# Kernel tuning notes

Hardware: AMD Instinct MI355X
Metric: run time of the kernel (lower is better)

Reference implementation:

```python
import jax, jax.numpy as jnp
import numpy as np

DIM = 1024
NUM_HEADS = 8
HEAD_DIM = 128
MAX_SEQ_LEN = 2048
ATTN_SCALE = 0.12
RMS_EPS = 1.1920929e-07  # torch float32 eps (F.rms_norm default)


def rms_norm(x):
    return x * jax.lax.rsqrt(jnp.mean(jnp.square(x), axis=-1, keepdims=True) + RMS_EPS)


def rope_tables(T):
    # angular_freq: (1/1024)**linspace(0,1,head_dim//4), padded with head_dim//4 zeros -> length head_dim//2
    af = (1.0 / 1024.0) ** np.linspace(0.0, 1.0, HEAD_DIM // 4, dtype=np.float32)
    af = np.concatenate([af, np.zeros(HEAD_DIM // 4, dtype=np.float32)])
    t = np.arange(T, dtype=np.float32)
    theta = np.einsum('i,j->ij', t, af)  # [T, head_dim//2]
    return jnp.asarray(np.cos(theta)), jnp.asarray(np.sin(theta))


def apply_rope(x_BTHD, cos, sin):
    # cos/sin: [T, head_dim//2] -> broadcast [1,T,1,hd//2]
    c = cos[None, :, None, :]
    s = sin[None, :, None, :]
    x1, x2 = jnp.split(x_BTHD, 2, axis=-1)
    y1 = x1 * c + x2 * s
    y2 = -x1 * s + x2 * c
    return jnp.concatenate([y1, y2], axis=-1)


def setup_inputs() -> dict:
    key = jax.random.key(0)
    k1, k2, k3, k4, k5 = jax.random.split(key, 5)
    B, T = 4, 2048
    hdim = NUM_HEADS * HEAD_DIM
    std = 0.5 * DIM ** (-0.5)
    bound = (3.0 ** 0.5) * std
    x = jax.random.normal(k1, (B, T, DIM), dtype=jnp.float32)
    ve = jax.random.normal(k2, (B, T, DIM), dtype=jnp.float32)
    sa_lambdas = jax.random.uniform(k3, (2,), dtype=jnp.float32)
    qkv_w = jax.random.uniform(k4, (3, hdim, DIM), dtype=jnp.float32, minval=-bound, maxval=bound)
    # original inits c_proj to zeros; use small random so the output is non-trivial
    c_proj_weight = jax.random.normal(k5, (DIM, hdim), dtype=jnp.float32) * 0.02
    return {"x": x, "ve": ve, "sa_lambdas": sa_lambdas, "qkv_w": qkv_w,
            "c_proj_weight": c_proj_weight}


def reference(x, ve, sa_lambdas, qkv_w, c_proj_weight):
    B, T, D = x.shape
    H, hd = NUM_HEADS, HEAD_DIM
    Wqkv = qkv_w.reshape(3 * H * hd, D)
    qkv = jnp.einsum('btd,ed->bte', x, Wqkv).reshape(B, T, 3 * H, hd)
    q, k, v = jnp.split(qkv, 3, axis=-2)  # each [B,T,H,hd]
    q, k = rms_norm(q), rms_norm(k)
    cos, sin = rope_tables(T)
    q, k = apply_rope(q, cos, sin), apply_rope(k, cos, sin)
    v = sa_lambdas[0] * v + sa_lambdas[1] * ve.reshape(B, T, H, hd)
    # [B,H,T,T] scores
    attn = jnp.einsum('bqhd,bkhd->bhqk', q, k) * ATTN_SCALE
    causal = jnp.triu(jnp.ones((T, T), dtype=bool), k=1)
    attn = jnp.where(causal[None, None], -jnp.inf, attn)
    attn = jax.nn.softmax(attn, axis=-1)
    y = jnp.einsum('bhqk,bkhd->bqhd', attn, v).reshape(B, T, H * hd)
    return jnp.einsum('bte,de->btd', y, c_proj_weight)
```

## Files before the change

kernel.cpp:

```cpp
#include <hip/hip_runtime.h>

#define DIM 1024
#define NH 8
#define HD 128
#define T_SEQ 2048
#define NTOK 8192
#define QKV_N 3072
#define ATTN_SCALE 0.12f
#define RMS_EPS 1.1920929e-07f

using f32x4  = __attribute__((ext_vector_type(4))) float;
using bf16x8 = __attribute__((ext_vector_type(8))) __bf16;

__device__ __forceinline__ unsigned short f2bf(float f) {
    unsigned int u = __builtin_bit_cast(unsigned int, f);
    u += 0x7fffu + ((u >> 16) & 1u);
    return (unsigned short)(u >> 16);
}
__device__ __forceinline__ float bf2f(unsigned short s) {
    unsigned int u = ((unsigned int)s) << 16;
    return __builtin_bit_cast(float, u);
}
__device__ __forceinline__ unsigned int cvtpk(float lo, float hi) {
    unsigned int r;
    asm("v_cvt_pk_bf16_f32 %0, %1, %2" : "=v"(r) : "v"(lo), "v"(hi));
    return r;
}

__device__ __forceinline__ void gll16(const void* g, void* l) {
    __builtin_amdgcn_global_load_lds(
        (const __attribute__((address_space(1))) unsigned int*)g,
        (__attribute__((address_space(3))) unsigned int*)l, 16, 0, 0);
}

#define VMCNT(n) asm volatile("s_waitcnt vmcnt(" #n ")" ::: "memory")
#define LGKM(n)  asm volatile("s_waitcnt lgkmcnt(" #n ")" ::: "memory")
#define LGKM0 do { asm volatile("s_waitcnt lgkmcnt(0)" ::: "memory"); \
                   __builtin_amdgcn_sched_barrier(0); } while(0)
#define PH_BAR __builtin_amdgcn_s_barrier()

__global__ __launch_bounds__(256) void prep(const float* __restrict__ x,
                                            const float* __restrict__ qkvw,
                                            const float* __restrict__ cprojw,
                                            unsigned short* __restrict__ xb,
                                            unsigned short* __restrict__ wqb,
                                            unsigned short* __restrict__ cpb,
                                            float2* __restrict__ tab) {
    const int bid = blockIdx.x;
    const int tid = threadIdx.x;
    if (bid < 12288) {
        const float* in;
        unsigned short* out;
        int i;
        if (bid < 8192)        { in = x;      out = xb;  i = bid*256 + tid; }
        else if (bid < 11264)  { in = qkvw;   out = wqb; i = (bid-8192)*256 + tid; }
        else                   { in = cprojw; out = cpb; i = (bid-11264)*256 + tid; }
        float4 f = ((const float4*)in)[i];
        ushort4 o;
        o.x = f2bf(f.x); o.y = f2bf(f.y); o.z = f2bf(f.z); o.w = f2bf(f.w);
        ((ushort4*)out)[i] = o;
    } else {
        int idx = (bid - 12288)*256 + tid;
        int t = idx >> 5, i = idx & 31;
        float th = (float)t * exp2f((float)i * (-10.0f/31.0f));
        float sn, cs;
        sincosf(th, &sn, &cs);
        tab[idx] = make_float2(cs, sn);
    }
}

template<int OUTF32>
__global__ __launch_bounds__(512, 2) void gemm8p(const unsigned short* __restrict__ A,
                                                 const unsigned short* __restrict__ B,
                                                 void* __restrict__ Cout,
                                                 int M, int N, int K, int nbn) {
    __shared__ __align__(16) char smem[139264];
    const int tid  = threadIdx.x;
    const int lane = tid & 63;
    const int w    = tid >> 6;
    const int wm   = w >> 2, wn = w & 3;
    const int lr   = lane & 15, lg = lane >> 4;

    const int chunk = gridDim.x >> 3;
    const int bid2  = (blockIdx.x & 7) * chunk + (blockIdx.x >> 3);
    const int bm = (bid2 / nbn) * 256;
    const int bn = (bid2 % nbn) * 256;

    const int rsub = lane >> 3;
    const int csw  = ((lane & 7) ^ rsub) << 3;
    const int KT = K / 64;

    auto stA = [&](int t, int h) {
        if (t >= KT) return;
        char* dst = smem + (t & 1) * 65536 + h * 16384;
        #pragma unroll
        for (int i = 0; i < 2; ++i) {
            int c = w*2 + i;
            gll16(&A[(size_t)(bm + h*128 + c*8 + rsub)*K + t*64 + csw], dst + c*1024);
        }
    };
    auto stB = [&](int t, int h) {
        if (t >= KT) return;
        char* dst = smem + (t & 1) * 65536 + 32768 + h * 16384;
        #pragma unroll
        for (int i = 0; i < 2; ++i) {
            int c = w*2 + i;
            gll16(&B[(size_t)(bn + h*128 + c*8 + rsub)*K + t*64 + csw], dst + c*1024);
        }
    };

    f32x4 acc[8][4] = {};
    bf16x8 a0[4][2], a1[4][2], bb[2][2];

    auto rdA = [&](int t, int qm, bf16x8 (*a)[2]) {
        const unsigned short* base = (const unsigned short*)(smem + (t & 1)*65536 + wm*16384);
        #pragma unroll
        for (int m = 0; m < 4; ++m) {
            int row = qm*64 + m*16 + lr;
            int sw = (row & 7) << 3;
            #pragma unroll
            for (int kk = 0; kk < 2; ++kk)
                a[m][kk] = *(const bf16x8*)&base[row*64 + ((kk*32 + lg*8) ^ sw)];
        }
    };
    auto rdB = [&](int t, int qn) {
        const unsigned short* base = (const unsigned short*)(smem + (t & 1)*65536 + 32768 + (wn >> 1)*16384);
        #pragma unroll
        for (int n = 0; n < 2; ++n) {
            int row = (wn & 1)*64 + qn*32 + n*16 + lr;
            int sw = (row & 7) << 3;
            #pragma unroll
            for (int kk = 0; kk < 2; ++kk)
                bb[n][kk] = *(const bf16x8*)&base[row*64 + ((kk*32 + lg*8) ^ sw)];
        }
    };
    auto mm = [&](bf16x8 (*a)[2], int qm, int qn) {
        __builtin_amdgcn_s_setprio(1);
        #pragma unroll
        for (int m = 0; m < 4; ++m)
            #pragma unroll
            for (int n = 0; n < 2; ++n)
                #pragma unroll
                for (int kk = 0; kk < 2; ++kk)
                    acc[qm*4+m][qn*2+n] =
                        __builtin_amdgcn_mfma_f32_16x16x32_bf16(a[m][kk], bb[n][kk],
                                                                acc[qm*4+m][qn*2+n], 0, 0, 0);
        __builtin_amdgcn_s_setprio(0);
    };

    stA(0, 0); stA(0, 1); stB(0, 0); stB(0, 1);
    stA(1, 0); stA(1, 1);
    VMCNT(4);
    PH_BAR;

    for (int t = 0; t < KT; ++t) {
        rdA(t, 0, a0); rdB(t, 0);
        stB(t + 1, 0);
        LGKM(8);
        PH_BAR; LGKM0;
        mm(a0, 0, 0);
        PH_BAR;
        rdA(t, 1, a1);
        stB(t + 1, 1);
        PH_BAR; LGKM0;
        mm(a1, 1, 0);
        PH_BAR;
        rdB(t, 1);
        stA(t + 2, 0);
        PH_BAR; LGKM0;
        mm(a0, 0, 1);
        PH_BAR;
        stA(t + 2, 1);
        if (t + 2 < KT) { VMCNT(4); } else { VMCNT(0); }
        PH_BAR;
        mm(a1, 1, 1);
        PH_BAR;
    }

    __syncthreads();
    float* sc = (float*)(smem + (size_t)w * 17408);
    #pragma unroll
    for (int f = 0; f < 2; ++f) {
        #pragma unroll
        for (int m = 0; m < 4; ++m)
            #pragma unroll
            for (int n = 0; n < 4; ++n)
                #pragma unroll
                for (int r = 0; r < 4; ++r)
                    sc[(m*16 + lg*4 + r)*68 + n*16 + lr] = acc[f*4+m][n][r];
        if (OUTF32) {
            float* C = (float*)Cout;
            #pragma unroll
            for (int rnd = 0; rnd < 16; ++rnd) {
                int g = rnd*64 + lane;
                int row = g >> 4, c4 = (g & 15) * 4;
                float4 v = *(float4*)&sc[row*68 + c4];
                *(float4*)&C[(size_t)(bm + wm*128 + f*64 + row)*N + bn + wn*64 + c4] = v;
            }
        } else {
            unsigned short* C = (unsigned short*)Cout;
            #pragma unroll
            for (int rnd = 0; rnd < 8; ++rnd) {
                int g = rnd*64 + lane;
                int row = g >> 3, c8 = (g & 7) * 8;
                float4 v0 = *(float4*)&sc[row*68 + c8];
                float4 v1 = *(float4*)&sc[row*68 + c8 + 4];
                uint4 o;
                o.x = f2bf(v0.x) | ((unsigned)f2bf(v0.y) << 16);
                o.y = f2bf(v0.z) | ((unsigned)f2bf(v0.w) << 16);
                o.z = f2bf(v1.x) | ((unsigned)f2bf(v1.y) << 16);
                o.w = f2bf(v1.z) | ((unsigned)f2bf(v1.w) << 16);
                *(uint4*)&C[(size_t)(bm + wm*128 + f*64 + row)*N + bn + wn*64 + c8] = o;
            }
        }
        if (f == 0) __syncthreads();
    }
}

#define SLOT_A 32768
#define SLOT_SZ 49152

template<int OUTF32>
__global__ __launch_bounds__(512, 1) void gemm256(const unsigned short* __restrict__ A,
                                                  const unsigned short* __restrict__ B,
                                                  void* __restrict__ Cout,
                                                  int M, int N, int K, int nbn) {
    __shared__ __align__(16) char smem[147456];
    const int tid  = threadIdx.x;
    const int lane = tid & 63;
    const int w    = tid >> 6;
    const int wm   = w >> 1, wn = w & 1;
    const int lr   = lane & 15, lg = lane >> 4;
    const int xsw  = (lr & 7) << 3;

    const int chunk = gridDim.x >> 3;
    const int bid2  = (blockIdx.x & 7) * chunk + (blockIdx.x >> 3);
    const int m0 = (bid2 / nbn) * 256;
    const int n0 = (bid2 % nbn) * 128;

    const int rsub = lane >> 3;
    const int csw  = ((lane & 7) ^ rsub) << 3;

    char* s0 = smem;
    char* s1 = smem + SLOT_SZ;
    char* s2 = smem + 2*SLOT_SZ;

    auto stage = [&](int kt, char* slot) {
        const int kb = kt * 64;
        #pragma unroll
        for (int i = 0; i < 4; ++i) {
            int c = w*4 + i;
            gll16(&A[(size_t)(m0 + c*8 + rsub)*K + kb + csw], slot + c*1024);
        }
        #pragma unroll
        for (int i = 0; i < 2; ++i) {
            int c = w*2 + i;
            gll16(&B[(size_t)(n0 + c*8 + rsub)*K + kb + csw], slot + SLOT_A + c*1024);
        }
    };

    f32x4 acc[4][4] = {};
    const int KT = K / 64;

    stage(0, s0);
    stage(1, s1);
    VMCNT(6);
    __builtin_amdgcn_s_barrier();
    __builtin_amdgcn_sched_barrier(0);

    for (int t = 0; t < KT; ++t) {
        if (t + 2 < KT) stage(t + 2, s2);
        const unsigned short* sA = (const unsigned short*)s0;
        const unsigned short* sB = (const unsigned short*)(s0 + SLOT_A);
        bf16x8 bfr[4][2];
        #pragma unroll
        for (int n = 0; n < 4; ++n)
            #pragma unroll
            for (int kk = 0; kk < 2; ++kk)
                bfr[n][kk] = *(const bf16x8*)&sB[(wn*64 + n*16 + lr)*64 + ((kk*32 + lg*8) ^ xsw)];
        #pragma unroll
        for (int m = 0; m < 4; ++m) {
            bf16x8 af[2];
            #pragma unroll
            for (int kk = 0; kk < 2; ++kk)
                af[kk] = *(const bf16x8*)&sA[(wm*64 + m*16 + lr)*64 + ((kk*32 + lg*8) ^ xsw)];
            __builtin_amdgcn_s_setprio(1);
            #pragma unroll
            for (int n = 0; n < 4; ++n)
                #pragma unroll
                for (int kk = 0; kk < 2; ++kk)
                    acc[m][n] = __builtin_amdgcn_mfma_f32_16x16x32_bf16(af[kk], bfr[n][kk], acc[m][n], 0, 0, 0);
            __builtin_amdgcn_s_setprio(0);
        }
        if (t + 2 < KT) { VMCNT(6); }
        else            { VMCNT(0); }
        __builtin_amdgcn_s_barrier();
        __builtin_amdgcn_sched_barrier(0);
        char* tmp = s0; s0 = s1; s1 = s2; s2 = tmp;
    }

    __syncthreads();
    float* sc = (float*)(smem + (size_t)w * 17408);
    #pragma unroll
    for (int m = 0; m < 4; ++m)
        #pragma unroll
        for (int n = 0; n < 4; ++n)
            #pragma unroll
            for (int r = 0; r < 4; ++r)
                sc[(m*16 + lg*4 + r)*68 + n*16 + lr] = acc[m][n][r];

    if (OUTF32) {
        float* Cg = (float*)Cout;
        #pragma unroll
        for (int rnd = 0; rnd < 16; ++rnd) {
            int g = rnd*64 + lane;
            int row = g >> 4, c4 = (g & 15) * 4;
            float4 v = *(float4*)&sc[row*68 + c4];
            *(float4*)&Cg[(size_t)(m0 + wm*64 + row)*N + n0 + wn*64 + c4] = v;
        }
    } else {
        unsigned short* Cg = (unsigned short*)Cout;
        #pragma unroll
        for (int rnd = 0; rnd < 8; ++rnd) {
            int g = rnd*64 + lane;
            int row = g >> 3, c8 = (g & 7) * 8;
            float4 v0 = *(float4*)&sc[row*68 + c8];
            float4 v1 = *(float4*)&sc[row*68 + c8 + 4];
            uint4 o;
            o.x = f2bf(v0.x) | ((unsigned)f2bf(v0.y) << 16);
            o.y = f2bf(v0.z) | ((unsigned)f2bf(v0.w) << 16);
            o.z = f2bf(v1.x) | ((unsigned)f2bf(v1.y) << 16);
            o.w = f2bf(v1.z) | ((unsigned)f2bf(v1.w) << 16);
            *(uint4*)&Cg[(size_t)(m0 + wm*64 + row)*N + n0 + wn*64 + c8] = o;
        }
    }
}

__global__ __launch_bounds__(256) void post(const unsigned short* __restrict__ qkv,
                                            const float* __restrict__ ve,
                                            const float* __restrict__ lam,
                                            const float2* __restrict__ tab,
                                            unsigned short* __restrict__ qO,
                                            unsigned short* __restrict__ kO,
                                            unsigned short* __restrict__ vt) {
    __shared__ unsigned short lT[128*72];
    const int bid = blockIdx.x;
    const int tid = threadIdx.x;
    if (bid < 16384) {
        int gw   = (bid*256 + tid) >> 6;
        int lane = tid & 63;
        int h     = gw & 7;
        int token = gw >> 3;
        int t     = token & (T_SEQ-1);
        int b     = token >> 11;

        const unsigned short* base = qkv + (size_t)token * QKV_N + h*HD;
        float q1 = bf2f(base[lane]),        q2 = bf2f(base[lane+64]);
        float k1 = bf2f(base[1024+lane]),   k2 = bf2f(base[1024+lane+64]);

        float sq = q1*q1 + q2*q2;
        float sk = k1*k1 + k2*k2;
        #pragma unroll
        for (int m = 1; m < 64; m <<= 1) {
            sq += __shfl_xor(sq, m);
            sk += __shfl_xor(sk, m);
        }
        float qs = rsqrtf(sq * (1.0f/128.0f) + RMS_EPS) * (ATTN_SCALE * 1.44269504088896f);
        float ks = rsqrtf(sk * (1.0f/128.0f) + RMS_EPS);
        q1 *= qs; q2 *= qs; k1 *= ks; k2 *= ks;

        float cs = 1.0f, sn = 0.0f;
        if (lane < 32) { float2 cc = tab[t*32 + lane]; cs = cc.x; sn = cc.y; }
        float qy1 =  q1*cs + q2*sn, qy2 = -q1*sn + q2*cs;
        float ky1 =  k1*cs + k2*sn, ky2 = -k1*sn + k2*cs;

        size_t obase = ((size_t)(b*NH + h) * T_SEQ + t) * HD;
        qO[obase + lane]      = f2bf(qy1);
        qO[obase + lane + 64] = f2bf(qy2);
        kO[obase + lane]      = f2bf(ky1);
        kO[obase + lane + 64] = f2bf(ky2);
    } else {
        const int idx = bid - 16384;
        const int t0  = (idx & 31) * 64;
        const int bh  = idx >> 5;
        const int b = bh >> 3, h = bh & 7;
        const float l0 = lam[0], l1 = lam[1];
        #pragma unroll
        for (int it = 0; it < 4; ++it) {
            int g  = it*256 + tid;
            int t  = g >> 4;
            int d8 = (g & 15) << 3;
            size_t token = (size_t)b*T_SEQ + t0 + t;
            ushort4 v0 = *(const ushort4*)&qkv[token*QKV_N + 2048 + h*HD + d8];
            ushort4 v1 = *(const ushort4*)&qkv[token*QKV_N + 2048 + h*HD + d8 + 4];
            float4 e0 = *(const float4*)&ve[token*DIM + h*HD + d8];
            float4 e1 = *(const float4*)&ve[token*DIM + h*HD + d8 + 4];
            lT[(d8+0)*72 + t] = f2bf(l0*bf2f(v0.x) + l1*e0.x);
            lT[(d8+1)*72 + t] = f2bf(l0*bf2f(v0.y) + l1*e0.y);
            lT[(d8+2)*72 + t] = f2bf(l0*bf2f(v0.z) + l1*e0.z);
            lT[(d8+3)*72 + t] = f2bf(l0*bf2f(v0.w) + l1*e0.w);
            lT[(d8+4)*72 + t] = f2bf(l0*bf2f(v1.x) + l1*e1.x);
            lT[(d8+5)*72 + t] = f2bf(l0*bf2f(v1.y) + l1*e1.y);
            lT[(d8+6)*72 + t] = f2bf(l0*bf2f(v1.z) + l1*e1.z);
            lT[(d8+7)*72 + t] = f2bf(l0*bf2f(v1.w) + l1*e1.w);
        }
        __syncthreads();
        #pragma unroll
        for (int it = 0; it < 4; ++it) {
            int g  = it*256 + tid;
            int d  = g >> 3;
            int t8 = (g & 7) << 3;
            uint4 pk = *(const uint4*)&lT[d*72 + t8];
            *(uint4*)&vt[((size_t)bh*HD + d)*T_SEQ + t0 + t8] = pk;
        }
    }
}

__global__ __launch_bounds__(256, 2) void attn_fwd(const unsigned short* __restrict__ Q,
                                                   const unsigned short* __restrict__ K,
                                                   const unsigned short* __restrict__ Vt,
                                                   unsigned short* __restrict__ Y) {
    __shared__ unsigned short lK[2][64*128];
    __shared__ unsigned short lV[2][128*64];
    __shared__ unsigned short lP[4][16*72];
    __shared__ float lden[4][2][16];

    const int tid  = threadIdx.x;
    const int lane = tid & 63;
    const int w    = tid >> 6;
    const int lr   = lane & 15, lg = lane >> 4;

    const int lin = blockIdx.y * 16 + blockIdx.x;
    const int bh  = (lin & 7)*4 + ((lin >> 3) & 3);
    const int p   = lin >> 5;
    const int qtA = p, qtB = 31 - p;

    const unsigned short* Qg = Q  + (size_t)bh * T_SEQ * HD;
    const unsigned short* Kg = K  + (size_t)bh * T_SEQ * HD;
    const unsigned short* Vg = Vt + (size_t)bh * HD * T_SEQ;
    const int q0A = qtA*64 + w*16;
    const int q0B = qtB*64 + w*16;

    auto stage = [&](int kt, int s) {
        const int kbase = kt * 64;
        #pragma unroll
        for (int i = 0; i < 4; ++i) {
            int c = w*4 + i;
            int row = c*4 + (lane >> 4);
            int col = ((lane & 15) << 3) ^ ((row & 7) << 3);
            gll16(&Kg[(size_t)(kbase + row)*HD + col], &lK[s][c*512]);
        }
        #pragma unroll
        for (int i = 0; i < 4; ++i) {
            int c = w*4 + i;
            int row = c*8 + (lane >> 3);
            int col = ((lane & 7) << 3) ^ ((row & 7) << 3);
            gll16(&Vg[(size_t)row*T_SEQ + kbase + col], &lV[s][c*512]);
        }
    };

    bf16x8 qfA[4], qfB[4];
    #pragma unroll
    for (int kk = 0; kk < 4; ++kk) {
        qfA[kk] = *(const bf16x8*)&Qg[(size_t)(q0A + lr)*HD + kk*32 + lg*8];
        qfB[kk] = *(const bf16x8*)&Qg[(size_t)(q0B + lr)*HD + kk*32 + lg*8];
    }
    VMCNT(0);
    #pragma unroll
    for (int kk = 0; kk < 4; ++kk)
        asm volatile("" :: "v"(qfA[kk]), "v"(qfB[kk]));

    f32x4 oA[8] = {}, oB[8] = {};
    float psA = 0.f, psB = 0.f;

    auto softmax_pack = [&](f32x4* sf, float& ps, uint2* pk) {
        #pragma unroll
        for (int j = 0; j < 4; ++j)
            #pragma unroll
            for (int r = 0; r < 4; ++r) {
                float pp = exp2f(sf[j][r]);
                sf[j][r] = pp;
                ps += pp;
            }
        #pragma unroll
        for (int j = 0; j < 4; ++j) {
            pk[j].x = cvtpk(sf[j][0], sf[j][1]);
            pk[j].y = cvtpk(sf[j][2], sf[j][3]);
        }
    };
    auto p_store = [&](uint2* pk) {
        #pragma unroll
        for (int j = 0; j < 4; ++j)
            *(uint2*)&lP[w][lr*72 + j*16 + lg*4] = pk[j];
        asm volatile("" ::: "memory");
    };

    auto passAB = [&](bool diagA, int kbase,
                      const unsigned short* lKc, const unsigned short* lVc) {
        f32x4 sfA[4], sfB[4];
        __builtin_amdgcn_s_setprio(1);
        #pragma unroll
        for (int j = 0; j < 4; ++j) {
            f32x4 sA = {0.f,0.f,0.f,0.f}, sB = {0.f,0.f,0.f,0.f};
            #pragma unroll
            for (int kk = 0; kk < 4; ++kk) {
                bf16x8 kf = *(const bf16x8*)&lKc[(j*16+lr)*128 + ((kk*32 + lg*8) ^ ((lr&7)<<3))];
                sA = __builtin_amdgcn_mfma_f32_16x16x32_bf16(kf, qfA[kk], sA, 0, 0, 0);
                sB = __builtin_amdgcn_mfma_f32_16x16x32_bf16(kf, qfB[kk], sB, 0, 0, 0);
            }
            sfA[j] = sA; sfB[j] = sB;
        }
        __builtin_amdgcn_s_setprio(0);
        if (diagA) {
            #pragma unroll
            for (int j = 0; j < 4; ++j)
                #pragma unroll
                for (int r = 0; r < 4; ++r) {
                    int kcol = kbase + j*16 + lg*4 + r;
                    int qrow = q0A + lr;
                    if (kcol > qrow) sfA[j][r] = -INFINITY;
                }
        }
        uint2 pkA[4], pkB[4];
        softmax_pack(sfA, psA, pkA);
        p_store(pkA);
        softmax_pack(sfB, psB, pkB);
        bf16x8 pfA[2];
        #pragma unroll
        for (int kk = 0; kk < 2; ++kk)
            pfA[kk] = *(const bf16x8*)&lP[w][lr*72 + kk*32 + lg*8];
        asm volatile("" ::: "memory");
        p_store(pkB);
        bf16x8 pfB[2];
        #pragma unroll
        for (int kk = 0; kk < 2; ++kk)
            pfB[kk] = *(const bf16x8*)&lP[w][lr*72 + kk*32 + lg*8];
        #pragma unroll
        for (int n = 0; n < 8; ++n) {
            bf16x8 vf0 = *(const bf16x8*)&lVc[(n*16+lr)*64 + (( 0 + lg*8) ^ ((lr&7)<<3))];
            bf16x8 vf1 = *(const bf16x8*)&lVc[(n*16+lr)*64 + ((32 + lg*8) ^ ((lr&7)<<3))];
            __builtin_amdgcn_s_setprio(1);
            oA[n] = __builtin_amdgcn_mfma_f32_16x16x32_bf16(pfA[0], vf0, oA[n], 0, 0, 0);
            oB[n] = __builtin_amdgcn_mfma_f32_16x16x32_bf16(pfB[0], vf0, oB[n], 0, 0, 0);
            oA[n] = __builtin_amdgcn_mfma_f32_16x16x32_bf16(pfA[1], vf1, oA[n], 0, 0, 0);
            oB[n] = __builtin_amdgcn_mfma_f32_16x16x32_bf16(pfB[1], vf1, oB[n], 0, 0, 0);
            __builtin_amdgcn_s_setprio(0);
        }
    };

    auto pass = [&](bool diag, int kbase,
                    const unsigned short* lKc, const unsigned short* lVc) {
        f32x4 sf[4];
        __builtin_amdgcn_s_setprio(1);
        #pragma unroll
        for (int j = 0; j < 4; ++j) {
            f32x4 s = {0.f,0.f,0.f,0.f};
            #pragma unroll
            for (int kk = 0; kk < 4; ++kk) {
                bf16x8 kf = *(const bf16x8*)&lKc[(j*16+lr)*128 + ((kk*32 + lg*8) ^ ((lr&7)<<3))];
                s = __builtin_amdgcn_mfma_f32_16x16x32_bf16(kf, qfB[kk], s, 0, 0, 0);
            }
            sf[j] = s;
        }
        __builtin_amdgcn_s_setprio(0);
        if (diag) {
            #pragma unroll
            for (int j = 0; j < 4; ++j)
                #pragma unroll
                for (int r = 0; r < 4; ++r) {
                    int kcol = kbase + j*16 + lg*4 + r;
                    int qrow = q0B + lr;
                    if (kcol > qrow) sf[j][r] = -INFINITY;
                }
        }
        uint2 pk[4];
        softmax_pack(sf, psB, pk);
        p_store(pk);
        bf16x8 pf[2];
        #pragma unroll
        for (int kk = 0; kk < 2; ++kk)
            pf[kk] = *(const bf16x8*)&lP[w][lr*72 + kk*32 + lg*8];
        #pragma unroll
        for (int n = 0; n < 8; ++n) {
            bf16x8 vf0 = *(const bf16x8*)&lVc[(n*16+lr)*64 + (( 0 + lg*8) ^ ((lr&7)<<3))];
            bf16x8 vf1 = *(const bf16x8*)&lVc[(n*16+lr)*64 + ((32 + lg*8) ^ ((lr&7)<<3))];
            __builtin_amdgcn_s_setprio(1);
            oB[n] = __builtin_amdgcn_mfma_f32_16x16x32_bf16(pf[0], vf0, oB[n], 0, 0, 0);
            oB[n] = __builtin_amdgcn_mfma_f32_16x16x32_bf16(pf[1], vf1, oB[n], 0, 0, 0);
            __builtin_amdgcn_s_setprio(0);
        }
    };

    stage(0, 0);
    for (int kt = 0; kt <= qtB; ++kt) {
        __builtin_amdgcn_s_barrier();
        const bool pre = (kt + 1 <= qtB);
        if (pre) stage(kt + 1, (kt + 1) & 1);
        if (pre) { VMCNT(8); } else { VMCNT(0); }
        __builtin_amdgcn_sched_barrier(0);
        const int kbase = kt * 64;
        const unsigned short* lKc = lK[kt & 1];
        const unsigned short* lVc = lV[kt & 1];
        if (kt <= qtA) passAB(kt == qtA, kbase, lKc, lVc);
        else           pass(kt == qtB, kbase, lKc, lVc);
    }

    psA += __shfl_xor(psA, 16); psA += __shfl_xor(psA, 32);
    psB += __shfl_xor(psB, 16); psB += __shfl_xor(psB, 32);
    if (lane < 16) { lden[w][0][lane] = psA; lden[w][1][lane] = psB; }
    asm volatile("" ::: "memory");
    float riA[4], riB[4];
    #pragma unroll
    for (int r = 0; r < 4; ++r) {
        riA[r] = 1.0f / lden[w][0][lg*4 + r];
        riB[r] = 1.0f / lden[w][1][lg*4 + r];
    }

    const int b = bh >> 3, h = bh & 7;
    #pragma unroll
    for (int n = 0; n < 8; ++n)
        #pragma unroll
        for (int r = 0; r < 4; ++r) {
            int d = n*16 + lr;
            int qrowA = q0A + lg*4 + r;
            int qrowB = q0B + lg*4 + r;
            Y[((size_t)(b*T_SEQ + qrowA))*DIM + h*HD + d] = f2bf(oA[n][r] * riA[r]);
            Y[((size_t)(b*T_SEQ + qrowB))*DIM + h*HD + d] = f2bf(oB[n][r] * riB[r]);
        }
}

extern "C" void kernel_launch(void* const* d_in, const int* in_sizes, int n_in,
                              void* d_out, int out_size, void* d_ws, size_t ws_size,
                              hipStream_t stream) {
    const float* x      = (const float*)d_in[0];
    const float* ve     = (const float*)d_in[1];
    const float* lam    = (const float*)d_in[2];
    const float* qkvw   = (const float*)d_in[3];
    const float* cprojw = (const float*)d_in[4];

    char* ws = (char*)d_ws;
    unsigned short* xb  = (unsigned short*)(ws);
    unsigned short* wqb = (unsigned short*)(ws + 16777216);
    unsigned short* cpb = (unsigned short*)(ws + 23068672);
    unsigned short* qkv = (unsigned short*)(ws + 25165824);
    unsigned short* qa  = (unsigned short*)(ws + 75497472);
    unsigned short* ka  = (unsigned short*)(ws + 92274688);
    unsigned short* vt  = (unsigned short*)(ws + 109051904);
    unsigned short* ya  = (unsigned short*)(ws + 125829120);
    float2* tab = (float2*)(ws + 142606336);

    prep<<<12544, 256, 0, stream>>>(x, qkvw, cprojw, xb, wqb, cpb, tab);

    gemm8p<0><<<384, 512, 0, stream>>>(xb, wqb, qkv, NTOK, QKV_N, DIM, 12);
    post<<<17408, 256, 0, stream>>>(qkv, ve, lam, tab, qa, ka, vt);
    attn_fwd<<<dim3(16, 32), 256, 0, stream>>>(qa, ka, vt, ya);
    gemm256<1><<<256, 512, 0, stream>>>(ya, cpb, (float*)d_out, NTOK, DIM, DIM, 8);
}
```

Before: 190.2 us.

## Stage K/V through registers into single LDS buffer to raise occupancy

Replaces the double-buffered direct global-to-LDS loads of K and V tiles with a single LDS buffer fed from register staging: the next tile is loaded into registers during compute and written to LDS after a barrier. This halves K/V shared memory so launch bounds are raised from 2 to 3 blocks per CU. It costs extra VGPRs for staging, two barriers per iteration, and serializes the LDS write with compute, and the tighter register budget may cause spills.

```diff
diff --git a/kernel.cpp b/kernel.cpp
--- a/kernel.cpp
+++ b/kernel.cpp
@@ -416,12 +416,12 @@
     }
 }
 
-__global__ __launch_bounds__(256, 2) void attn_fwd(const unsigned short* __restrict__ Q,
+__global__ __launch_bounds__(256, 3) void attn_fwd(const unsigned short* __restrict__ Q,
                                                    const unsigned short* __restrict__ K,
                                                    const unsigned short* __restrict__ Vt,
                                                    unsigned short* __restrict__ Y) {
-    __shared__ unsigned short lK[2][64*128];
-    __shared__ unsigned short lV[2][128*64];
+    __shared__ unsigned short lK[64*128];
+    __shared__ unsigned short lV[128*64];
     __shared__ unsigned short lP[4][16*72];
     __shared__ float lden[4][2][16];
 
@@ -441,22 +441,36 @@
     const int q0A = qtA*64 + w*16;
     const int q0B = qtB*64 + w*16;
 
-    auto stage = [&](int kt, int s) {
+    uint4 kst[4], vst[4];
+    auto loadRegs = [&](int kt) {
         const int kbase = kt * 64;
         #pragma unroll
         for (int i = 0; i < 4; ++i) {
             int c = w*4 + i;
             int row = c*4 + (lane >> 4);
             int col = ((lane & 15) << 3) ^ ((row & 7) << 3);
-            gll16(&Kg[(size_t)(kbase + row)*HD + col], &lK[s][c*512]);
+            kst[i] = *(const uint4*)&Kg[(size_t)(kbase + row)*HD + col];
         }
         #pragma unroll
         for (int i = 0; i < 4; ++i) {
             int c = w*4 + i;
             int row = c*8 + (lane >> 3);
             int col = ((lane & 7) << 3) ^ ((row & 7) << 3);
-            gll16(&Vg[(size_t)row*T_SEQ + kbase + col], &lV[s][c*512]);
-        }
+            vst[i] = *(const uint4*)&Vg[(size_t)row*T_SEQ + kbase + col];
+        }
+    };
+    auto writeRegs = [&]() {
+        #pragma unroll
+        for (int i = 0; i < 4; ++i) {
+            int c = w*4 + i;
+            *(uint4*)&lK[c*512 + lane*8] = kst[i];
+        }
+        #pragma unroll
+        for (int i = 0; i < 4; ++i) {
+            int c = w*4 + i;
+            *(uint4*)&lV[c*512 + lane*8] = vst[i];
+        }
+        asm volatile("" ::: "memory");
     };
 
     bf16x8 qfA[4], qfB[4];
@@ -495,8 +509,7 @@
         asm volatile("" ::: "memory");
     };
 
-    auto passAB = [&](bool diagA, int kbase,
-                      const unsigned short* lKc, const unsigned short* lVc) {
+    auto passAB = [&](bool diagA, int kbase) {
         f32x4 sfA[4], sfB[4];
         __builtin_amdgcn_s_setprio(1);
         #pragma unroll
@@ -504,7 +517,7 @@
             f32x4 sA = {0.f,0.f,0.f,0.f}, sB = {0.f,0.f,0.f,0.f};
             #pragma unroll
             for (int kk = 0; kk < 4; ++kk) {
-                bf16x8 kf = *(const bf16x8*)&lKc[(j*16+lr)*128 + ((kk*32 + lg*8) ^ ((lr&7)<<3))];
+                bf16x8 kf = *(const bf16x8*)&lK[(j*16+lr)*128 + ((kk*32 + lg*8) ^ ((lr&7)<<3))];
                 sA = __builtin_amdgcn_mfma_f32_16x16x32_bf16(kf, qfA[kk], sA, 0, 0, 0);
                 sB = __builtin_amdgcn_mfma_f32_16x16x32_bf16(kf, qfB[kk], sB, 0, 0, 0);
             }
@@ -537,8 +550,8 @@
             pfB[kk] = *(const bf16x8*)&lP[w][lr*72 + kk*32 + lg*8];
         #pragma unroll
         for (int n = 0; n < 8; ++n) {
-            bf16x8 vf0 = *(const bf16x8*)&lVc[(n*16+lr)*64 + (( 0 + lg*8) ^ ((lr&7)<<3))];
-            bf16x8 vf1 = *(const bf16x8*)&lVc[(n*16+lr)*64 + ((32 + lg*8) ^ ((lr&7)<<3))];
+            bf16x8 vf0 = *(const bf16x8*)&lV[(n*16+lr)*64 + (( 0 + lg*8) ^ ((lr&7)<<3))];
+            bf16x8 vf1 = *(const bf16x8*)&lV[(n*16+lr)*64 + ((32 + lg*8) ^ ((lr&7)<<3))];
             __builtin_amdgcn_s_setprio(1);
             oA[n] = __builtin_amdgcn_mfma_f32_16x16x32_bf16(pfA[0], vf0, oA[n], 0, 0, 0);
             oB[n] = __builtin_amdgcn_mfma_f32_16x16x32_bf16(pfB[0], vf0, oB[n], 0, 0, 0);
@@ -548,8 +561,7 @@
         }
     };
 
-    auto pass = [&](bool diag, int kbase,
-                    const unsigned short* lKc, const unsigned short* lVc) {
+    auto pass = [&](bool diag, int kbase) {
         f32x4 sf[4];
         __builtin_amdgcn_s_setprio(1);
         #pragma unroll
@@ -557,7 +569,7 @@
             f32x4 s = {0.f,0.f,0.f,0.f};
             #pragma unroll
             for (int kk = 0; kk < 4; ++kk) {
-                bf16x8 kf = *(const bf16x8*)&lKc[(j*16+lr)*128 + ((kk*32 + lg*8) ^ ((lr&7)<<3))];
+                bf16x8 kf = *(const bf16x8*)&lK[(j*16+lr)*128 + ((kk*32 + lg*8) ^ ((lr&7)<<3))];
                 s = __builtin_amdgcn_mfma_f32_16x16x32_bf16(kf, qfB[kk], s, 0, 0, 0);
             }
             sf[j] = s;
@@ -582,8 +594,8 @@
             pf[kk] = *(const bf16x8*)&lP[w][lr*72 + kk*32 + lg*8];
         #pragma unroll
         for (int n = 0; n < 8; ++n) {
-            bf16x8 vf0 = *(const bf16x8*)&lVc[(n*16+lr)*64 + (( 0 + lg*8) ^ ((lr&7)<<3))];
-            bf16x8 vf1 = *(const bf16x8*)&lVc[(n*16+lr)*64 + ((32 + lg*8) ^ ((lr&7)<<3))];
+            bf16x8 vf0 = *(const bf16x8*)&lV[(n*16+lr)*64 + (( 0 + lg*8) ^ ((lr&7)<<3))];
+            bf16x8 vf1 = *(const bf16x8*)&lV[(n*16+lr)*64 + ((32 + lg*8) ^ ((lr&7)<<3))];
             __builtin_amdgcn_s_setprio(1);
             oB[n] = __builtin_amdgcn_mfma_f32_16x16x32_bf16(pf[0], vf0, oB[n], 0, 0, 0);
             oB[n] = __builtin_amdgcn_mfma_f32_16x16x32_bf16(pf[1], vf1, oB[n], 0, 0, 0);
@@ -591,18 +603,26 @@
         }
     };
 
-    stage(0, 0);
+    loadRegs(0);
+    writeRegs();
+    loadRegs(1);
+    LGKM0;
+    PH_BAR;
+    __builtin_amdgcn_sched_barrier(0);
+
     for (int kt = 0; kt <= qtB; ++kt) {
-        __builtin_amdgcn_s_barrier();
-        const bool pre = (kt + 1 <= qtB);
-        if (pre) stage(kt + 1, (kt + 1) & 1);
-        if (pre) { VMCNT(8); } else { VMCNT(0); }
+        const int kbase = kt * 64;
+        if (kt <= qtA) passAB(kt == qtA, kbase);
+        else           pass(kt == qtB, kbase);
+        PH_BAR;
         __builtin_amdgcn_sched_barrier(0);
-        const int kbase = kt * 64;
-        const unsigned short* lKc = lK[kt & 1];
-        const unsigned short* lVc = lV[kt & 1];
-        if (kt <= qtA) passAB(kt == qtA, kbase, lKc, lVc);
-        else           pass(kt == qtB, kbase, lKc, lVc);
+        if (kt + 1 <= qtB) {
+            writeRegs();
+            if (kt + 2 <= qtB) loadRegs(kt + 2);
+            LGKM0;
+        }
+        PH_BAR;
+        __builtin_amdgcn_sched_barrier(0);
     }
 
     psA += __shfl_xor(psA, 16); psA += __shfl_xor(psA, 32);
```

Result: slower. 406.1 us (+113.5%).

## Replace 256x256 QKV GEMM with 256x128 tile kernel and more blocks

Applied to the files above, without the earlier changes.

The QKV projection GEMM moves from a 256x256 output tile with an 8-phase schedule to a 256x128 tile with a 2-phase schedule, doubling the grid from 384 to 768 blocks. Each wave now holds a 64x64 accumulator instead of 128x64, which cuts register pressure and shared memory per block. The aim is to fill the GPU's CUs better and cut tail imbalance, at the cost of lower arithmetic intensity and more re-reads of A from global memory. The epilogue is reworked to stage 16-row slices through a smaller shared buffer.

```diff
diff --git a/kernel.cpp b/kernel.cpp
--- a/kernel.cpp
+++ b/kernel.cpp
@@ -69,72 +69,73 @@
     }
 }
 
-template<int OUTF32>
-__global__ __launch_bounds__(512, 2) void gemm8p(const unsigned short* __restrict__ A,
+#define G2_SLOT 49152
+
+__global__ __launch_bounds__(512, 1) void gemm2p(const unsigned short* __restrict__ A,
                                                  const unsigned short* __restrict__ B,
-                                                 void* __restrict__ Cout,
+                                                 unsigned short* __restrict__ Cout,
                                                  int M, int N, int K, int nbn) {
-    __shared__ __align__(16) char smem[139264];
+    __shared__ __align__(16) char smem[98304];
     const int tid  = threadIdx.x;
     const int lane = tid & 63;
     const int w    = tid >> 6;
-    const int wm   = w >> 2, wn = w & 3;
+    const int wm   = w >> 1, wn = w & 1;
     const int lr   = lane & 15, lg = lane >> 4;
 
     const int chunk = gridDim.x >> 3;
     const int bid2  = (blockIdx.x & 7) * chunk + (blockIdx.x >> 3);
     const int bm = (bid2 / nbn) * 256;
-    const int bn = (bid2 % nbn) * 256;
+    const int bn = (bid2 % nbn) * 128;
 
     const int rsub = lane >> 3;
     const int csw  = ((lane & 7) ^ rsub) << 3;
     const int KT = K / 64;
 
-    auto stA = [&](int t, int h) {
+    auto stA = [&](int t) {
         if (t >= KT) return;
-        char* dst = smem + (t & 1) * 65536 + h * 16384;
+        char* dst = smem + (t & 1) * G2_SLOT;
+        #pragma unroll
+        for (int i = 0; i < 4; ++i) {
+            int c = w*4 + i;
+            gll16(&A[(size_t)(bm + c*8 + rsub)*K + t*64 + csw], dst + c*1024);
+        }
+    };
+    auto stB = [&](int t) {
+        if (t >= KT) return;
+        char* dst = smem + (t & 1) * G2_SLOT + 32768;
         #pragma unroll
         for (int i = 0; i < 2; ++i) {
             int c = w*2 + i;
-            gll16(&A[(size_t)(bm + h*128 + c*8 + rsub)*K + t*64 + csw], dst + c*1024);
-        }
-    };
-    auto stB = [&](int t, int h) {
-        if (t >= KT) return;
-        char* dst = smem + (t & 1) * 65536 + 32768 + h * 16384;
-        #pragma unroll
-        for (int i = 0; i < 2; ++i) {
-            int c = w*2 + i;
-            gll16(&B[(size_t)(bn + h*128 + c*8 + rsub)*K + t*64 + csw], dst + c*1024);
-        }
-    };
-
-    f32x4 acc[8][4] = {};
-    bf16x8 a0[4][2], a1[4][2], bb[2][2];
-
-    auto rdA = [&](int t, int qm, bf16x8 (*a)[2]) {
-        const unsigned short* base = (const unsigned short*)(smem + (t & 1)*65536 + wm*16384);
+            gll16(&B[(size_t)(bn + c*8 + rsub)*K + t*64 + csw], dst + c*1024);
+        }
+    };
+
+    f32x4 acc[4][4] = {};
+    bf16x8 a[4][2], bb[2][2];
+
+    auto rdA = [&](int t) {
+        const unsigned short* base = (const unsigned short*)(smem + (t & 1)*G2_SLOT);
         #pragma unroll
         for (int m = 0; m < 4; ++m) {
-            int row = qm*64 + m*16 + lr;
+            int row = wm*64 + m*16 + lr;
             int sw = (row & 7) << 3;
             #pragma unroll
             for (int kk = 0; kk < 2; ++kk)
                 a[m][kk] = *(const bf16x8*)&base[row*64 + ((kk*32 + lg*8) ^ sw)];
         }
     };
-    auto rdB = [&](int t, int qn) {
-        const unsigned short* base = (const unsigned short*)(smem + (t & 1)*65536 + 32768 + (wn >> 1)*16384);
+    auto rdB = [&](int t, int half) {
+        const unsigned short* base = (const unsigned short*)(smem + (t & 1)*G2_SLOT + 32768);
         #pragma unroll
         for (int n = 0; n < 2; ++n) {
-            int row = (wn & 1)*64 + qn*32 + n*16 + lr;
+            int row = wn*64 + half*32 + n*16 + lr;
             int sw = (row & 7) << 3;
             #pragma unroll
             for (int kk = 0; kk < 2; ++kk)
                 bb[n][kk] = *(const bf16x8*)&base[row*64 + ((kk*32 + lg*8) ^ sw)];
         }
     };
-    auto mm = [&](bf16x8 (*a)[2], int qm, int qn) {
+    auto mm = [&](int qn) {
         __builtin_amdgcn_s_setprio(1);
         #pragma unroll
         for (int m = 0; m < 4; ++m)
@@ -142,78 +143,53 @@
             for (int n = 0; n < 2; ++n)
                 #pragma unroll
                 for (int kk = 0; kk < 2; ++kk)
-                    acc[qm*4+m][qn*2+n] =
+                    acc[m][qn*2+n] =
                         __builtin_amdgcn_mfma_f32_16x16x32_bf16(a[m][kk], bb[n][kk],
-                                                                acc[qm*4+m][qn*2+n], 0, 0, 0);
+                                                                acc[m][qn*2+n], 0, 0, 0);
         __builtin_amdgcn_s_setprio(0);
     };
 
-    stA(0, 0); stA(0, 1); stB(0, 0); stB(0, 1);
-    stA(1, 0); stA(1, 1);
+    stA(0); stB(0); stA(1);
     VMCNT(4);
     PH_BAR;
 
     for (int t = 0; t < KT; ++t) {
-        rdA(t, 0, a0); rdB(t, 0);
-        stB(t + 1, 0);
+        rdA(t); rdB(t, 0);
+        stB(t + 1);
         LGKM(8);
         PH_BAR; LGKM0;
-        mm(a0, 0, 0);
-        PH_BAR;
-        rdA(t, 1, a1);
-        stB(t + 1, 1);
-        PH_BAR; LGKM0;
-        mm(a1, 1, 0);
+        mm(0);
         PH_BAR;
         rdB(t, 1);
-        stA(t + 2, 0);
+        stA(t + 2);
+        if (t + 2 < KT) { VMCNT(4); } else { VMCNT(0); }
         PH_BAR; LGKM0;
-        mm(a0, 0, 1);
+        mm(1);
         PH_BAR;
-        stA(t + 2, 1);
-        if (t + 2 < KT) { VMCNT(4); } else { VMCNT(0); }
-        PH_BAR;
-        mm(a1, 1, 1);
-        PH_BAR;
     }
 
     __syncthreads();
-    float* sc = (float*)(smem + (size_t)w * 17408);
+    float* sc = (float*)(smem + (size_t)w * 4352);
     #pragma unroll
-    for (int f = 0; f < 2; ++f) {
-        #pragma unroll
-        for (int m = 0; m < 4; ++m)
-            #pragma unroll
-            for (int n = 0; n < 4; ++n)
-                #pragma unroll
-                for (int r = 0; r < 4; ++r)
-                    sc[(m*16 + lg*4 + r)*68 + n*16 + lr] = acc[f*4+m][n][r];
-        if (OUTF32) {
-            float* C = (float*)Cout;
-            #pragma unroll
-            for (int rnd = 0; rnd < 16; ++rnd) {
-                int g = rnd*64 + lane;
-                int row = g >> 4, c4 = (g & 15) * 4;
-                float4 v = *(float4*)&sc[row*68 + c4];
-                *(float4*)&C[(size_t)(bm + wm*128 + f*64 + row)*N + bn + wn*64 + c4] = v;
-            }
-        } else {
-            unsigned short* C = (unsigned short*)Cout;
-            #pragma unroll
-            for (int rnd = 0; rnd < 8; ++rnd) {
-                int g = rnd*64 + lane;
-                int row = g >> 3, c8 = (g & 7) * 8;
-                float4 v0 = *(float4*)&sc[row*68 + c8];
-                float4 v1 = *(float4*)&sc[row*68 + c8 + 4];
-                uint4 o;
-                o.x = f2bf(v0.x) | ((unsigned)f2bf(v0.y) << 16);
-                o.y = f2bf(v0.z) | ((unsigned)f2bf(v0.w) << 16);
-                o.z = f2bf(v1.x) | ((unsigned)f2bf(v1.y) << 16);
-                o.w = f2bf(v1.z) | ((unsigned)f2bf(v1.w) << 16);
-                *(uint4*)&C[(size_t)(bm + wm*128 + f*64 + row)*N + bn + wn*64 + c8] = o;
-            }
-        }
-        if (f == 0) __syncthreads();
+    for (int m = 0; m < 4; ++m) {
+        #pragma unroll
+        for (int nn = 0; nn < 4; ++nn)
+            #pragma unroll
+            for (int r = 0; r < 4; ++r)
+                sc[(lg*4 + r)*68 + nn*16 + lr] = acc[m][nn][r];
+        #pragma unroll
+        for (int rnd = 0; rnd < 2; ++rnd) {
+            int g = rnd*64 + lane;
+            int row = g >> 3, c8 = (g & 7) * 8;
+            float4 v0 = *(float4*)&sc[row*68 + c8];
+            float4 v1 = *(float4*)&sc[row*68 + c8 + 4];
+            uint4 o;
+            o.x = f2bf(v0.x) | ((unsigned)f2bf(v0.y) << 16);
+            o.y = f2bf(v0.z) | ((unsigned)f2bf(v0.w) << 16);
+            o.z = f2bf(v1.x) | ((unsigned)f2bf(v1.y) << 16);
+            o.w = f2bf(v1.z) | ((unsigned)f2bf(v1.w) << 16);
+            *(uint4*)&Cout[(size_t)(bm + wm*64 + m*16 + row)*N + bn + wn*64 + c8] = o;
+        }
     }
 }
 
@@ -651,7 +627,7 @@
 
     prep<<<12544, 256, 0, stream>>>(x, qkvw, cprojw, xb, wqb, cpb, tab);
 
-    gemm8p<0><<<384, 512, 0, stream>>>(xb, wqb, qkv, NTOK, QKV_N, DIM, 12);
+    gemm2p<<<768, 512, 0, stream>>>(xb, wqb, qkv, NTOK, QKV_N, DIM, 24);
     post<<<17408, 256, 0, stream>>>(qkv, ve, lam, tab, qa, ka, vt);
     attn_fwd<<<dim3(16, 32), 256, 0, stream>>>(qa, ka, vt, ya);
     gemm256<1><<<256, 512, 0, stream>>>(ya, cpb, (float*)d_out, NTOK, DIM, DIM, 8);
```

Result: no change. 191.5 us (+0.7%).

## Merge two query-tile pairs per 512-thread attention block to share K/V staging

Applied to the files above, without the earlier changes.

The attention kernel now runs 512 threads per block, and each block handles two adjacent balanced query-tile pairs. The two halves of the block share each staged K/V tile, so the global-to-LDS traffic per query row is halved and each wave issues half as many staging loads. The P scratch buffer is also changed from a padded stride of 72 to an XOR-swizzled stride of 64 to avoid bank conflicts, and the denominator buffer is folded into it after a sync. In exchange, half the waves idle on the last key tile, the grid shrinks to 256 blocks, and the launch bound claims 4 blocks per CU, which may limit registers.

```diff
diff --git a/kernel.cpp b/kernel.cpp
--- a/kernel.cpp
+++ b/kernel.cpp
@@ -416,43 +416,44 @@
     }
 }
 
-__global__ __launch_bounds__(256, 2) void attn_fwd(const unsigned short* __restrict__ Q,
+__global__ __launch_bounds__(512, 4) void attn_fwd(const unsigned short* __restrict__ Q,
                                                    const unsigned short* __restrict__ K,
                                                    const unsigned short* __restrict__ Vt,
                                                    unsigned short* __restrict__ Y) {
     __shared__ unsigned short lK[2][64*128];
     __shared__ unsigned short lV[2][128*64];
-    __shared__ unsigned short lP[4][16*72];
-    __shared__ float lden[4][2][16];
+    __shared__ unsigned short lP[8][16*64];
 
     const int tid  = threadIdx.x;
     const int lane = tid & 63;
     const int w    = tid >> 6;
     const int lr   = lane & 15, lg = lane >> 4;
 
-    const int lin = blockIdx.y * 16 + blockIdx.x;
+    const int lin = blockIdx.y * 8 + blockIdx.x;
     const int bh  = (lin & 7)*4 + ((lin >> 3) & 3);
-    const int p   = lin >> 5;
-    const int qtA = p, qtB = 31 - p;
+    const int i2  = lin >> 5;
+    const int p0  = i2*2 + (w >> 2);
+    const int qtA = p0, qtB = 31 - p0;
+    const int kmax = 31 - i2*2;
 
     const unsigned short* Qg = Q  + (size_t)bh * T_SEQ * HD;
     const unsigned short* Kg = K  + (size_t)bh * T_SEQ * HD;
     const unsigned short* Vg = Vt + (size_t)bh * HD * T_SEQ;
-    const int q0A = qtA*64 + w*16;
-    const int q0B = qtB*64 + w*16;
+    const int q0A = qtA*64 + (w & 3)*16;
+    const int q0B = qtB*64 + (w & 3)*16;
 
     auto stage = [&](int kt, int s) {
         const int kbase = kt * 64;
         #pragma unroll
-        for (int i = 0; i < 4; ++i) {
-            int c = w*4 + i;
+        for (int i = 0; i < 2; ++i) {
+            int c = w*2 + i;
             int row = c*4 + (lane >> 4);
             int col = ((lane & 15) << 3) ^ ((row & 7) << 3);
             gll16(&Kg[(size_t)(kbase + row)*HD + col], &lK[s][c*512]);
         }
         #pragma unroll
-        for (int i = 0; i < 4; ++i) {
-            int c = w*4 + i;
+        for (int i = 0; i < 2; ++i) {
+            int c = w*2 + i;
             int row = c*8 + (lane >> 3);
             int col = ((lane & 7) << 3) ^ ((row & 7) << 3);
             gll16(&Vg[(size_t)row*T_SEQ + kbase + col], &lV[s][c*512]);
@@ -491,7 +492,7 @@
     auto p_store = [&](uint2* pk) {
         #pragma unroll
         for (int j = 0; j < 4; ++j)
-            *(uint2*)&lP[w][lr*72 + j*16 + lg*4] = pk[j];
+            *(uint2*)&lP[w][lr*64 + ((j*16 + lg*4) ^ ((lr & 7) << 3))] = pk[j];
         asm volatile("" ::: "memory");
     };
 
@@ -528,13 +529,13 @@
         bf16x8 pfA[2];
         #pragma unroll
         for (int kk = 0; kk < 2; ++kk)
-            pfA[kk] = *(const bf16x8*)&lP[w][lr*72 + kk*32 + lg*8];
+            pfA[kk] = *(const bf16x8*)&lP[w][lr*64 + ((kk*32 + lg*8) ^ ((lr&7)<<3))];
         asm volatile("" ::: "memory");
         p_store(pkB);
         bf16x8 pfB[2];
         #pragma unroll
         for (int kk = 0; kk < 2; ++kk)
-            pfB[kk] = *(const bf16x8*)&lP[w][lr*72 + kk*32 + lg*8];
+            pfB[kk] = *(const bf16x8*)&lP[w][lr*64 + ((kk*32 + lg*8) ^ ((lr&7)<<3))];
         #pragma unroll
         for (int n = 0; n < 8; ++n) {
             bf16x8 vf0 = *(const bf16x8*)&lVc[(n*16+lr)*64 + (( 0 + lg*8) ^ ((lr&7)<<3))];
@@ -579,7 +580,7 @@
         bf16x8 pf[2];
         #pragma unroll
         for (int kk = 0; kk < 2; ++kk)
-            pf[kk] = *(const bf16x8*)&lP[w][lr*72 + kk*32 + lg*8];
+            pf[kk] = *(const bf16x8*)&lP[w][lr*64 + ((kk*32 + lg*8) ^ ((lr&7)<<3))];
         #pragma unroll
         for (int n = 0; n < 8; ++n) {
             bf16x8 vf0 = *(const bf16x8*)&lVc[(n*16+lr)*64 + (( 0 + lg*8) ^ ((lr&7)<<3))];
@@ -592,28 +593,30 @@
     };
 
     stage(0, 0);
-    for (int kt = 0; kt <= qtB; ++kt) {
+    for (int kt = 0; kt <= kmax; ++kt) {
         __builtin_amdgcn_s_barrier();
-        const bool pre = (kt + 1 <= qtB);
+        const bool pre = (kt + 1 <= kmax);
         if (pre) stage(kt + 1, (kt + 1) & 1);
-        if (pre) { VMCNT(8); } else { VMCNT(0); }
+        if (pre) { VMCNT(4); } else { VMCNT(0); }
         __builtin_amdgcn_sched_barrier(0);
         const int kbase = kt * 64;
         const unsigned short* lKc = lK[kt & 1];
         const unsigned short* lVc = lV[kt & 1];
-        if (kt <= qtA) passAB(kt == qtA, kbase, lKc, lVc);
-        else           pass(kt == qtB, kbase, lKc, lVc);
-    }
-
+        if (kt <= qtA)      passAB(kt == qtA, kbase, lKc, lVc);
+        else if (kt <= qtB) pass(kt == qtB, kbase, lKc, lVc);
+    }
+
+    __syncthreads();
+    float* ld = (float*)&lP[0][0];
     psA += __shfl_xor(psA, 16); psA += __shfl_xor(psA, 32);
     psB += __shfl_xor(psB, 16); psB += __shfl_xor(psB, 32);
-    if (lane < 16) { lden[w][0][lane] = psA; lden[w][1][lane] = psB; }
+    if (lane < 16) { ld[w*32 + lane] = psA; ld[w*32 + 16 + lane] = psB; }
     asm volatile("" ::: "memory");
     float riA[4], riB[4];
     #pragma unroll
     for (int r = 0; r < 4; ++r) {
-        riA[r] = 1.0f / lden[w][0][lg*4 + r];
-        riB[r] = 1.0f / lden[w][1][lg*4 + r];
+        riA[r] = 1.0f / ld[w*32 + lg*4 + r];
+        riB[r] = 1.0f / ld[w*32 + 16 + lg*4 + r];
     }
 
     const int b = bh >> 3, h = bh & 7;
@@ -653,6 +656,6 @@
 
     gemm8p<0><<<384, 512, 0, stream>>>(xb, wqb, qkv, NTOK, QKV_N, DIM, 12);
     post<<<17408, 256, 0, stream>>>(qkv, ve, lam, tab, qa, ka, vt);
-    attn_fwd<<<dim3(16, 32), 256, 0, stream>>>(qa, ka, vt, ya);
+    attn_fwd<<<dim3(8, 32), 512, 0, stream>>>(qa, ka, vt, ya);
     gemm256<1><<<256, 512, 0, stream>>>(ya, cpb, (float*)d_out, NTOK, DIM, DIM, 8);
 }
```

New measurement: 271.0 us. 42.5% more time.
